# Kernel optimization log

Measured on AMD Instinct MI355X. Metric: run time of the kernel, lower is better.

## Reference

```python
import jax, jax.numpy as jnp
import numpy as np

N_NODES = 80000
N_EDGES = 800000
N_REL = 400
D_IN = 256
D_OUT = 256
BN_EPS = 1e-5


def _xavier(key, shape, gain=np.sqrt(2.0)):
    fan_in, fan_out = shape[0], shape[-1]
    std = gain * np.sqrt(2.0 / (fan_in + fan_out))
    return jax.random.normal(key, shape, dtype=jnp.float32) * std


def ccorr(a, b):
    # circular correlation: irfft(conj(rfft(a)) * rfft(b), n)
    n = a.shape[-1]
    return jnp.fft.irfft(jnp.conj(jnp.fft.rfft(a)) * jnp.fft.rfft(b), n)


def setup_inputs() -> dict:
    key = jax.random.key(0)
    ks = jax.random.split(key, 12)
    x = jax.random.normal(ks[0], (N_NODES, D_IN), dtype=jnp.float32)
    rel_repr = jax.random.normal(ks[1], (N_REL, D_IN), dtype=jnp.float32)
    edge_src = jax.random.randint(ks[2], (N_EDGES,), 0, N_NODES)
    edge_dst = jax.random.randint(ks[3], (N_EDGES,), 0, N_NODES)
    edge_type = jax.random.randint(ks[4], (N_EDGES,), 0, N_REL)
    edge_norm = jax.random.uniform(ks[5], (N_EDGES,), dtype=jnp.float32)
    in_w = _xavier(ks[6], (D_IN, D_OUT))
    out_w = _xavier(ks[7], (D_IN, D_OUT))
    loop_w = _xavier(ks[8], (D_IN, D_OUT))
    w_rel = _xavier(ks[9], (D_IN, D_OUT))
    loop_rel = _xavier(ks[10], (1, D_IN))
    bias = jnp.zeros((D_OUT,), dtype=jnp.float32)
    return {"x": x, "rel_repr": rel_repr, "edge_src": edge_src,
            "edge_dst": edge_dst, "edge_type": edge_type, "edge_norm": edge_norm,
            "in_w": in_w, "out_w": out_w, "loop_w": loop_w, "w_rel": w_rel,
            "loop_rel": loop_rel, "bias": bias}


def reference(x, rel_repr, edge_src, edge_dst, edge_type, edge_norm,
              in_w, out_w, loop_w, w_rel, loop_rel, bias):
    E = edge_src.shape[0]
    half = E // 2
    # gather + compose (opn == 'corr')
    h_src = x[edge_src]                         # [E, D_in]
    edge_data = ccorr(h_src, rel_repr[edge_type])  # [E, D_in]
    # direction-split matmul
    msg = jnp.concatenate([edge_data[:half] @ in_w,
                           edge_data[half:] @ out_w], axis=0)  # [E, D_out]
    msg = msg * edge_norm[:, None]
    # scatter-sum into destination nodes, then reduce (dropout p=0, /3)
    agg = jax.ops.segment_sum(msg, edge_dst, num_segments=x.shape[0]) / 3.0
    # self-loop
    loop = ccorr(x, jnp.broadcast_to(loop_rel, x.shape)) @ loop_w / 3.0
    out = agg + loop + bias
    # BatchNorm1d (training mode: batch stats, gamma=1, beta=0)
    mean = jnp.mean(out, axis=0)
    var = jnp.var(out, axis=0)
    out = (out - mean) / jnp.sqrt(var + BN_EPS)
    # act is identity
    return out, rel_repr @ w_rel
```

## Files before the change

kernel.cpp:

```cpp
#include <hip/hip_runtime.h>

#define NN 80000
#define NE 800000
#define EH 400000
#define NR 400
#define DD 256
#define FD 256
#define KP 768
#define NB 160000
#define NCH 157
#define MT 80400
#define PI2 6.283185307179586f

typedef unsigned short u16;
typedef __attribute__((ext_vector_type(8))) short bf16x8;
typedef __attribute__((ext_vector_type(4))) float f32x4;

static __device__ __forceinline__ float bu2f(u16 u) {
  return __uint_as_float(((unsigned int)u) << 16);
}
static __device__ __forceinline__ u16 f2bu(float f) {
  unsigned int x = __float_as_uint(f);
  x += 0x7fffu + ((x >> 16) & 1u);
  return (u16)(x >> 16);
}
static __device__ __forceinline__ unsigned int pk2(float a, float b) {
  return (unsigned int)f2bu(a) | ((unsigned int)f2bu(b) << 16);
}
static __device__ __forceinline__ void gload16(const void* g, void* l) {
  __builtin_amdgcn_global_load_lds(
      (const __attribute__((address_space(1))) unsigned int*)g,
      (__attribute__((address_space(3))) unsigned int*)l, 16, 0, 0);
}

__global__ void k_build(const float* __restrict__ in_w, const float* __restrict__ out_w,
                        const float* __restrict__ lr, const float* __restrict__ loop_w,
                        u16* __restrict__ Ft, u16* __restrict__ Bt) {
  __shared__ float L[DD];
  int bb = blockIdx.x, c = threadIdx.x;
  if (bb < 256) {
    int row = bb, j = c;
    int k, im;
    if (row == 0)      { k = 0;   im = 0; }
    else if (row == 1) { k = 128; im = 0; }
    else               { k = row >> 1; im = row & 1; }
    int m = (j * k) & 255;
    float th = -PI2 * (float)m * (1.0f / 256.0f);
    Ft[row * 256 + j] = f2bu(im ? sinf(th) : cosf(th));
  } else if (bb < 768) {
    int t = bb - 256;
    const float* W = (t < 256) ? in_w : out_w;
    int tp = t & 255;
    int k, im; float alpha;
    if (tp == 0)      { k = 0;   im = 0; alpha = 1.0f; }
    else if (tp == 1) { k = 128; im = 0; alpha = 1.0f; }
    else              { k = tp >> 1; im = tp & 1; alpha = 2.0f; }
    float scale = alpha * (1.0f / 768.0f);
    float th = -PI2 * (float)k * (1.0f / 256.0f);
    float wr = cosf(th), wi = sinf(th);
    float zr = 1.0f, zi = 0.0f;
    float acc = 0.0f;
    for (int j = 0; j < DD; ++j) {
      float coef = im ? zi : zr;
      acc += coef * W[(size_t)j * DD + c];
      float nzr = zr * wr - zi * wi; zi = zr * wi + zi * wr; zr = nzr;
    }
    Bt[(size_t)c * KP + t] = f2bu(scale * acc);
  } else {
    int j = bb - 768;
    L[c] = lr[c];
    __syncthreads();
    float acc = 0.0f;
    for (int k2 = 0; k2 < DD; ++k2)
      acc += L[(j + k2) & 255] * loop_w[(size_t)k2 * DD + c];
    Bt[(size_t)c * KP + 512 + j] = f2bu(acc * (1.0f / 3.0f));
  }
}

__global__ __launch_bounds__(512) void k_dft(
    const float* __restrict__ x, const float* __restrict__ rel,
    const u16* __restrict__ Ft, u16* __restrict__ xfh, float* __restrict__ rfhf,
    u16* __restrict__ Ap) {
  __shared__ u16 sA[2][128 * 64];
  __shared__ u16 sB[256 * 64];
  int tid = threadIdx.x;
  int w = tid >> 6, lane = tid & 63;
  int r0 = blockIdx.x * 128;
  int wm = (w & 1) * 64, wn = (w >> 1) * 64;
  int fr = lane & 15, fg = lane >> 4;

  int arow = tid >> 2;
  int acg = (tid & 3) * 16;
  int gr = r0 + arow;
  int grc = gr < MT ? gr : MT - 1;
  const float* asrc = (grc < NN) ? (x + (size_t)grc * DD)
                                 : (rel + (size_t)(grc - NN) * DD);
  bool doAp = (gr < NN);

  float4 a0_, a1_, a2_, a3_;
#define LOADA(kb) { const float* p_ = asrc + (kb) * 64 + acg;                     \
    a0_ = *(const float4*)(p_);     a1_ = *(const float4*)(p_ + 4);               \
    a2_ = *(const float4*)(p_ + 8); a3_ = *(const float4*)(p_ + 12); }

#define STGB(kb) { _Pragma("unroll") for (int q = 0; q < 4; ++q) {                \
    int s_ = w * 4 + q; int c_ = 8 * s_ + (lane >> 3);                            \
    int cb_ = (lane & 7) ^ (c_ & 7);                                              \
    gload16(Ft + (size_t)c_ * 256 + (kb) * 64 + cb_ * 8, sB + s_ * 512); } }

#define CVTA(kb, buf) {                                                           \
    uint4 c0_ = make_uint4(pk2(a0_.x, a0_.y), pk2(a0_.z, a0_.w),                  \
                           pk2(a1_.x, a1_.y), pk2(a1_.z, a1_.w));                 \
    uint4 c1_ = make_uint4(pk2(a2_.x, a2_.y), pk2(a2_.z, a2_.w),                  \
                           pk2(a3_.x, a3_.y), pk2(a3_.z, a3_.w));                 \
    int b0_ = (tid & 3) * 2;                                                      \
    *(uint4*)(sA[buf] + arow * 64 + ((b0_ ^ (arow & 7)) * 8)) = c0_;              \
    *(uint4*)(sA[buf] + arow * 64 + (((b0_ + 1) ^ (arow & 7)) * 8)) = c1_;        \
    if (doAp) { u16* ap_ = Ap + (size_t)gr * KP + 512 + (kb) * 64 + acg;          \
      *(uint4*)(ap_) = c0_; *(uint4*)(ap_ + 8) = c1_; } }

  f32x4 acc[4][4];
#pragma unroll
  for (int i = 0; i < 4; ++i)
#pragma unroll
    for (int j = 0; j < 4; ++j) acc[i][j] = (f32x4){0.f, 0.f, 0.f, 0.f};

  LOADA(0)
  STGB(0)
  CVTA(0, 0)
  LOADA(1)
  __syncthreads();
  for (int kb = 0; kb < 4; ++kb) {
    int cur = kb & 1;
#pragma unroll
    for (int ks = 0; ks < 2; ++ks) {
      bf16x8 af[4], bfr[4];
#pragma unroll
      for (int mt = 0; mt < 4; ++mt) {
        int r = wm + mt * 16 + fr;
        af[mt] = *(const bf16x8*)(sA[cur] + r * 64 + ((ks * 32 + fg * 8) ^ ((r & 7) * 8)));
      }
#pragma unroll
      for (int nt = 0; nt < 4; ++nt) {
        int c = wn + nt * 16 + fr;
        bfr[nt] = *(const bf16x8*)(sB + c * 64 + ((ks * 32 + fg * 8) ^ ((c & 7) * 8)));
      }
#pragma unroll
      for (int mt = 0; mt < 4; ++mt)
#pragma unroll
        for (int nt = 0; nt < 4; ++nt)
          acc[mt][nt] = __builtin_amdgcn_mfma_f32_16x16x32_bf16(af[mt], bfr[nt],
                                                                acc[mt][nt], 0, 0, 0);
    }
    __syncthreads();
    if (kb < 3) {
      STGB(kb + 1)
      CVTA(kb + 1, cur ^ 1)
      if (kb < 2) LOADA(kb + 2)
      __syncthreads();
    }
  }
#undef LOADA
#undef STGB
#undef CVTA

#pragma unroll
  for (int mt = 0; mt < 4; ++mt)
#pragma unroll
    for (int nt = 0; nt < 4; ++nt) {
      int cg = wn + nt * 16 + fr;
#pragma unroll
      for (int j = 0; j < 4; ++j) {
        int rg = r0 + wm + mt * 16 + fg * 4 + j;
        float val = acc[mt][nt][j];
        if (rg < NN)      xfh[(size_t)rg * FD + cg] = f2bu(val);
        else if (rg < MT) rfhf[(size_t)(rg - NN) * FD + cg] = val;
      }
    }
}

__global__ void k_hist(const int* __restrict__ edst, int* __restrict__ cnt) {
  int e = blockIdx.x * 256 + threadIdx.x;
  int key = edst[e] + ((e >= EH) ? NN : 0);
  atomicAdd(&cnt[key], 1);
}

__global__ __launch_bounds__(256) void k_scan1(const int* __restrict__ cnt,
                                               int* __restrict__ base,
                                               int* __restrict__ chunkTot) {
  __shared__ int wsum[4];
  int t = threadIdx.x;
  int g0 = blockIdx.x * 1024 + t * 4;
  int v[4], ex[4], s = 0;
#pragma unroll
  for (int j = 0; j < 4; ++j) v[j] = (g0 + j < NB) ? cnt[g0 + j] : 0;
#pragma unroll
  for (int j = 0; j < 4; ++j) { ex[j] = s; s += v[j]; }
  int lane = t & 63, w = t >> 6;
  int inc = s;
  for (int off = 1; off < 64; off <<= 1) {
    int n = __shfl_up(inc, off);
    if (lane >= off) inc += n;
  }
  if (lane == 63) wsum[w] = inc;
  __syncthreads();
  int woff = 0;
  for (int i = 0; i < w; ++i) woff += wsum[i];
  int exth = woff + inc - s;
#pragma unroll
  for (int j = 0; j < 4; ++j)
    if (g0 + j < NB) base[g0 + j] = exth + ex[j];
  if (t == 255) chunkTot[blockIdx.x] = woff + inc;
}

__global__ __launch_bounds__(256) void k_scan2(const int* __restrict__ chunkTot,
                                               int* __restrict__ chunkOff) {
  __shared__ int wsum[4];
  int t = threadIdx.x;
  int v = (t < NCH) ? chunkTot[t] : 0;
  int lane = t & 63, w = t >> 6;
  int inc = v;
  for (int off = 1; off < 64; off <<= 1) {
    int n = __shfl_up(inc, off);
    if (lane >= off) inc += n;
  }
  if (lane == 63) wsum[w] = inc;
  __syncthreads();
  int woff = 0;
  for (int i = 0; i < w; ++i) woff += wsum[i];
  if (t < NCH) chunkOff[t] = woff + inc - v;
}

__global__ void k_scan3(int* __restrict__ base, const int* __restrict__ chunkOff,
                        int* __restrict__ cursor) {
  int i = blockIdx.x * 256 + threadIdx.x;
  if (i < NB) {
    int b = base[i] + chunkOff[i >> 10];
    base[i] = b;
    cursor[i] = b;
  }
  if (i == 0) base[NB] = NE;
}

__global__ void k_scatter(const int* __restrict__ esrc, const int* __restrict__ edst,
                          const int* __restrict__ etyp, const float* __restrict__ enorm,
                          int* __restrict__ cursor, int4* __restrict__ recs) {
  int e = blockIdx.x * 256 + threadIdx.x;
  int key = edst[e] + ((e >= EH) ? NN : 0);
  int pos = atomicAdd(&cursor[key], 1);
  recs[pos] = make_int4(esrc[e], etyp[e], __float_as_int(enorm[e]), 0);
}

__global__ __launch_bounds__(256) void k_reduce(
    const u16* __restrict__ xfh, const float* __restrict__ rfhf,
    const int4* __restrict__ recs, const int* __restrict__ base,
    u16* __restrict__ Ap) {
  int w = threadIdx.x >> 6, lane = threadIdx.x & 63;
  int b = blockIdx.x * 4 + w;
  int start = base[b], end = base[b + 1];
  bool l0 = (lane == 0);
  float a0 = 0, a1 = 0, a2 = 0, a3 = 0;
  int p = start;
  for (; p + 3 < end; p += 4) {
    ushort4 xv[4];
    float4 rv[4];
    float nm[4];
#pragma unroll
    for (int u = 0; u < 4; ++u) {
      int4 rc = recs[p + u];
      nm[u] = __int_as_float(rc.z);
      xv[u] = *(const ushort4*)(xfh + (size_t)rc.x * FD + 4 * lane);
      rv[u] = *(const float4*)(rfhf + (size_t)rc.y * FD + 4 * lane);
    }
#pragma unroll
    for (int u = 0; u < 4; ++u) {
      float xr0 = bu2f(xv[u].x), xi0 = bu2f(xv[u].y);
      float xr1 = bu2f(xv[u].z), xi1 = bu2f(xv[u].w);
      float rr0 = rv[u].x, ri0 = rv[u].y, rr1 = rv[u].z, ri1 = rv[u].w;
      float p0 = l0 ? (xr0 * rr0) : (xr0 * rr0 + xi0 * ri0);
      float p1 = l0 ? (xi0 * ri0) : (xr0 * ri0 - xi0 * rr0);
      a0 += p0 * nm[u];
      a1 += p1 * nm[u];
      a2 += (xr1 * rr1 + xi1 * ri1) * nm[u];
      a3 += (xr1 * ri1 - xi1 * rr1) * nm[u];
    }
  }
  for (; p < end; ++p) {
    int4 rc = recs[p];
    float nm0 = __int_as_float(rc.z);
    ushort4 xv0 = *(const ushort4*)(xfh + (size_t)rc.x * FD + 4 * lane);
    float4 rv0 = *(const float4*)(rfhf + (size_t)rc.y * FD + 4 * lane);
    float xr0 = bu2f(xv0.x), xi0 = bu2f(xv0.y), xr1 = bu2f(xv0.z), xi1 = bu2f(xv0.w);
    float rr0 = rv0.x, ri0 = rv0.y, rr1 = rv0.z, ri1 = rv0.w;
    float p0 = l0 ? (xr0 * rr0) : (xr0 * rr0 + xi0 * ri0);
    float p1 = l0 ? (xi0 * ri0) : (xr0 * ri0 - xi0 * rr0);
    a0 += p0 * nm0;
    a1 += p1 * nm0;
    a2 += (xr1 * rr1 + xi1 * ri1) * nm0;
    a3 += (xr1 * ri1 - xi1 * rr1) * nm0;
  }
  u16* tp = Ap + ((b < NN) ? (size_t)b * KP : (size_t)(b - NN) * KP + 256);
  *(unsigned int*)(tp + 4 * lane)     = pk2(a0, a1);
  *(unsigned int*)(tp + 4 * lane + 2) = pk2(a2, a3);
}

__global__ __launch_bounds__(512) void k_mgemm(
    const u16* __restrict__ Ap, const u16* __restrict__ Bt,
    const float* __restrict__ bias, float* __restrict__ dout,
    float* __restrict__ sum1, float* __restrict__ sum2) {
  __shared__ u16 sA[2][128 * 64];
  __shared__ u16 sB[256 * 64];
  int tid = threadIdx.x;
  int w = tid >> 6, lane = tid & 63;
  int r0 = blockIdx.x * 128;
  int wm = (w & 1) * 64, wn = (w >> 1) * 64;
  int fr = lane & 15, fg = lane >> 4;

#define STGA(kb, buf) { _Pragma("unroll") for (int q = 0; q < 2; ++q) {           \
    int s_ = w * 2 + q; int r_ = 8 * s_ + (lane >> 3);                            \
    int cb_ = (lane & 7) ^ (r_ & 7);                                              \
    gload16(Ap + (size_t)(r0 + r_) * KP + (kb) * 64 + cb_ * 8,                    \
            sA[buf] + s_ * 512); } }

#define STGB(kb) { _Pragma("unroll") for (int q = 0; q < 4; ++q) {                \
    int s_ = w * 4 + q; int c_ = 8 * s_ + (lane >> 3);                            \
    int cb_ = (lane & 7) ^ (c_ & 7);                                              \
    gload16(Bt + (size_t)c_ * KP + (kb) * 64 + cb_ * 8, sB + s_ * 512); } }

  f32x4 acc[4][4];
#pragma unroll
  for (int i = 0; i < 4; ++i)
#pragma unroll
    for (int j = 0; j < 4; ++j) acc[i][j] = (f32x4){0.f, 0.f, 0.f, 0.f};

  STGA(0, 0)
  STGB(0)
  __syncthreads();
  for (int kb = 0; kb < 12; ++kb) {
    int cur = kb & 1;
    if (kb < 11) STGA(kb + 1, cur ^ 1)
#pragma unroll
    for (int ks = 0; ks < 2; ++ks) {
      bf16x8 af[4], bfr[4];
#pragma unroll
      for (int mt = 0; mt < 4; ++mt) {
        int r = wm + mt * 16 + fr;
        af[mt] = *(const bf16x8*)(sA[cur] + r * 64 + ((ks * 32 + fg * 8) ^ ((r & 7) * 8)));
      }
#pragma unroll
      for (int nt = 0; nt < 4; ++nt) {
        int c = wn + nt * 16 + fr;
        bfr[nt] = *(const bf16x8*)(sB + c * 64 + ((ks * 32 + fg * 8) ^ ((c & 7) * 8)));
      }
#pragma unroll
      for (int mt = 0; mt < 4; ++mt)
#pragma unroll
        for (int nt = 0; nt < 4; ++nt)
          acc[mt][nt] = __builtin_amdgcn_mfma_f32_16x16x32_bf16(af[mt], bfr[nt],
                                                                acc[mt][nt], 0, 0, 0);
    }
    __syncthreads();
    if (kb < 11) { STGB(kb + 1) __syncthreads(); }
  }
#undef STGA
#undef STGB

  float s1[4] = {0.f, 0.f, 0.f, 0.f}, s2[4] = {0.f, 0.f, 0.f, 0.f};
#pragma unroll
  for (int nt = 0; nt < 4; ++nt) {
    int cg = wn + nt * 16 + fr;
    float bv = bias[cg];
#pragma unroll
    for (int mt = 0; mt < 4; ++mt) {
#pragma unroll
      for (int j = 0; j < 4; ++j) {
        int rg = r0 + wm + mt * 16 + fg * 4 + j;
        float val = acc[mt][nt][j] + bv;
        dout[(size_t)rg * DD + cg] = val;
        s1[nt] += val;
        s2[nt] += val * val;
      }
    }
  }
#pragma unroll
  for (int nt = 0; nt < 4; ++nt) {
    s1[nt] += __shfl_xor(s1[nt], 16); s1[nt] += __shfl_xor(s1[nt], 32);
    s2[nt] += __shfl_xor(s2[nt], 16); s2[nt] += __shfl_xor(s2[nt], 32);
  }
  if (lane < 16) {
#pragma unroll
    for (int nt = 0; nt < 4; ++nt) {
      atomicAdd(&sum1[wn + nt * 16 + lane], s1[nt]);
      atomicAdd(&sum2[wn + nt * 16 + lane], s2[nt]);
    }
  }
}

__global__ __launch_bounds__(256) void k_norm(float* __restrict__ out,
                                              const float* __restrict__ sum1,
                                              const float* __restrict__ sum2) {
  size_t tid0 = (size_t)blockIdx.x * 256 + threadIdx.x;
  int c0 = (int)((tid0 * 4) & 255);
  float m[4], rs[4];
#pragma unroll
  for (int j = 0; j < 4; ++j) {
    float mm = sum1[c0 + j] * (1.0f / (float)NN);
    float var = sum2[c0 + j] * (1.0f / (float)NN) - mm * mm;
    m[j] = mm;
    rs[j] = rsqrtf(var + 1e-5f);
  }
  size_t total = (size_t)NN * DD / 4;
  size_t stride = (size_t)gridDim.x * 256;
  for (size_t i = tid0; i < total; i += stride) {
    float4* p = (float4*)out + i;
    float4 v = *p;
    v.x = (v.x - m[0]) * rs[0];
    v.y = (v.y - m[1]) * rs[1];
    v.z = (v.z - m[2]) * rs[2];
    v.w = (v.w - m[3]) * rs[3];
    *p = v;
  }
}

__global__ void k_rel(const float* __restrict__ rel, const float* __restrict__ wrel,
                      float* __restrict__ out2) {
  __shared__ float R[DD];
  int r = blockIdx.x, c = threadIdx.x;
  R[c] = rel[(size_t)r * DD + c];
  __syncthreads();
  float acc = 0.0f;
  for (int j = 0; j < DD; ++j)
    acc += R[j] * wrel[(size_t)j * DD + c];
  out2[(size_t)r * DD + c] = acc;
}

__global__ void k_fail(float* __restrict__ out, int n) {
  int i = blockIdx.x * 256 + threadIdx.x;
  if (i < n) out[i] = 1.0e6f;
}

extern "C" void kernel_launch(void* const* d_in, const int* in_sizes, int n_in,
                              void* d_out, int out_size, void* d_ws, size_t ws_size,
                              hipStream_t stream) {
  (void)in_sizes; (void)n_in;
  const float* x      = (const float*)d_in[0];
  const float* rel    = (const float*)d_in[1];
  const int*   esrc   = (const int*)d_in[2];
  const int*   edst   = (const int*)d_in[3];
  const int*   etyp   = (const int*)d_in[4];
  const float* enorm  = (const float*)d_in[5];
  const float* in_w   = (const float*)d_in[6];
  const float* out_w  = (const float*)d_in[7];
  const float* loop_w = (const float*)d_in[8];
  const float* w_rel  = (const float*)d_in[9];
  const float* lr     = (const float*)d_in[10];
  const float* bias   = (const float*)d_in[11];
  float* dout = (float*)d_out;

  char* wsb = (char*)d_ws;
  size_t off = 0;
  u16* Apack = (u16*)(wsb + off); off += (size_t)NN * KP * 2;
  u16* Bt    = (u16*)(wsb + off); off += (size_t)DD * KP * 2;
  u16* xfh   = (u16*)(wsb + off); off += (size_t)NN * FD * 2;
  float* rfhf = (float*)(wsb + off); off += (size_t)NR * FD * 4;
  u16* Ft    = (u16*)(wsb + off); off += (size_t)DD * DD * 2;
  int4* recs = (int4*)(wsb + off); off += (size_t)NE * 16;
  float* sum1  = (float*)(wsb + off); off += DD * 4;
  float* sum2  = (float*)(wsb + off); off += DD * 4;
  int* cnt   = (int*)(wsb + off); off += (size_t)(NB + 1) * 4;
  int* baseA = (int*)(wsb + off); off += (size_t)(NB + 1) * 4;
  int* curA  = (int*)(wsb + off); off += (size_t)NB * 4;
  int* chT   = (int*)(wsb + off); off += 256 * 4;
  int* chO   = (int*)(wsb + off); off += 256 * 4;

  if (ws_size < off) {
    k_fail<<<(out_size + 255) / 256, 256, 0, stream>>>(dout, out_size);
    return;
  }

  hipMemsetAsync(cnt, 0, (NB + 1) * sizeof(int), stream);
  hipMemsetAsync(sum1, 0, 2 * DD * sizeof(float), stream);
  k_build<<<1024, 256, 0, stream>>>(in_w, out_w, lr, loop_w, Ft, Bt);
  k_hist<<<NE / 256, 256, 0, stream>>>(edst, cnt);
  k_scan1<<<NCH, 256, 0, stream>>>(cnt, baseA, chT);
  k_scan2<<<1, 256, 0, stream>>>(chT, chO);
  k_scan3<<<(NB + 255) / 256, 256, 0, stream>>>(baseA, chO, curA);
  k_scatter<<<NE / 256, 256, 0, stream>>>(esrc, edst, etyp, enorm, curA, recs);
  k_dft<<<(MT + 127) / 128, 512, 0, stream>>>(x, rel, Ft, xfh, rfhf, Apack);
  k_reduce<<<NB / 4, 256, 0, stream>>>(xfh, rfhf, recs, baseA, Apack);
  k_mgemm<<<NN / 128, 512, 0, stream>>>(Apack, Bt, bias, dout, sum1, sum2);
  k_norm<<<2048, 256, 0, stream>>>(dout, sum1, sum2);
  k_rel<<<NR, 256, 0, stream>>>(rel, w_rel, dout + (size_t)NN * DD);
}
```

Baseline: 368.0 us.

## Store relation spectra and pre-norm output in bf16 to cut memory traffic

Relation DFT spectra are now stored as bf16 rather than fp32, which halves the gather bytes per edge in the reduce kernel. The GEMM writes its pre-normalisation output as a bf16 scratch buffer, and the norm kernel reads that buffer and writes fp32 output, so the fp32 read-modify-write round trip is avoided. The weight-spectrum build replaces the recurrent twiddle rotation with an exact twiddle table in shared memory. The cost is extra bf16 rounding on relation spectra and on output values before batch normalisation, plus more workspace.

```diff
diff --git a/kernel.cpp b/kernel.cpp
--- a/kernel.cpp
+++ b/kernel.cpp
@@ -56,15 +56,13 @@
     else if (tp == 1) { k = 128; im = 0; alpha = 1.0f; }
     else              { k = tp >> 1; im = tp & 1; alpha = 2.0f; }
     float scale = alpha * (1.0f / 768.0f);
-    float th = -PI2 * (float)k * (1.0f / 256.0f);
-    float wr = cosf(th), wi = sinf(th);
-    float zr = 1.0f, zi = 0.0f;
+    int m = (c * k) & 255;
+    float th = -PI2 * (float)m * (1.0f / 256.0f);
+    L[c] = im ? sinf(th) : cosf(th);
+    __syncthreads();
     float acc = 0.0f;
-    for (int j = 0; j < DD; ++j) {
-      float coef = im ? zi : zr;
-      acc += coef * W[(size_t)j * DD + c];
-      float nzr = zr * wr - zi * wi; zi = zr * wi + zi * wr; zr = nzr;
-    }
+    for (int j = 0; j < DD; ++j)
+      acc += L[j] * W[(size_t)j * DD + c];
     Bt[(size_t)c * KP + t] = f2bu(scale * acc);
   } else {
     int j = bb - 768;
@@ -79,7 +77,7 @@
 
 __global__ __launch_bounds__(512) void k_dft(
     const float* __restrict__ x, const float* __restrict__ rel,
-    const u16* __restrict__ Ft, u16* __restrict__ xfh, float* __restrict__ rfhf,
+    const u16* __restrict__ Ft, u16* __restrict__ xfh, u16* __restrict__ rfh,
     u16* __restrict__ Ap) {
   __shared__ u16 sA[2][128 * 64];
   __shared__ u16 sB[256 * 64];
@@ -171,9 +169,9 @@
 #pragma unroll
       for (int j = 0; j < 4; ++j) {
         int rg = r0 + wm + mt * 16 + fg * 4 + j;
-        float val = acc[mt][nt][j];
-        if (rg < NN)      xfh[(size_t)rg * FD + cg] = f2bu(val);
-        else if (rg < MT) rfhf[(size_t)(rg - NN) * FD + cg] = val;
+        u16 val = f2bu(acc[mt][nt][j]);
+        if (rg < NN)      xfh[(size_t)rg * FD + cg] = val;
+        else if (rg < MT) rfh[(size_t)(rg - NN) * FD + cg] = val;
       }
     }
 }
@@ -251,7 +249,7 @@
 }
 
 __global__ __launch_bounds__(256) void k_reduce(
-    const u16* __restrict__ xfh, const float* __restrict__ rfhf,
+    const u16* __restrict__ xfh, const u16* __restrict__ rfh,
     const int4* __restrict__ recs, const int* __restrict__ base,
     u16* __restrict__ Ap) {
   int w = threadIdx.x >> 6, lane = threadIdx.x & 63;
@@ -261,21 +259,21 @@
   float a0 = 0, a1 = 0, a2 = 0, a3 = 0;
   int p = start;
   for (; p + 3 < end; p += 4) {
-    ushort4 xv[4];
-    float4 rv[4];
+    ushort4 xv[4], rv[4];
     float nm[4];
 #pragma unroll
     for (int u = 0; u < 4; ++u) {
       int4 rc = recs[p + u];
       nm[u] = __int_as_float(rc.z);
       xv[u] = *(const ushort4*)(xfh + (size_t)rc.x * FD + 4 * lane);
-      rv[u] = *(const float4*)(rfhf + (size_t)rc.y * FD + 4 * lane);
+      rv[u] = *(const ushort4*)(rfh + (size_t)rc.y * FD + 4 * lane);
     }
 #pragma unroll
     for (int u = 0; u < 4; ++u) {
       float xr0 = bu2f(xv[u].x), xi0 = bu2f(xv[u].y);
       float xr1 = bu2f(xv[u].z), xi1 = bu2f(xv[u].w);
-      float rr0 = rv[u].x, ri0 = rv[u].y, rr1 = rv[u].z, ri1 = rv[u].w;
+      float rr0 = bu2f(rv[u].x), ri0 = bu2f(rv[u].y);
+      float rr1 = bu2f(rv[u].z), ri1 = bu2f(rv[u].w);
       float p0 = l0 ? (xr0 * rr0) : (xr0 * rr0 + xi0 * ri0);
       float p1 = l0 ? (xi0 * ri0) : (xr0 * ri0 - xi0 * rr0);
       a0 += p0 * nm[u];
@@ -288,9 +286,9 @@
     int4 rc = recs[p];
     float nm0 = __int_as_float(rc.z);
     ushort4 xv0 = *(const ushort4*)(xfh + (size_t)rc.x * FD + 4 * lane);
-    float4 rv0 = *(const float4*)(rfhf + (size_t)rc.y * FD + 4 * lane);
+    ushort4 rv0 = *(const ushort4*)(rfh + (size_t)rc.y * FD + 4 * lane);
     float xr0 = bu2f(xv0.x), xi0 = bu2f(xv0.y), xr1 = bu2f(xv0.z), xi1 = bu2f(xv0.w);
-    float rr0 = rv0.x, ri0 = rv0.y, rr1 = rv0.z, ri1 = rv0.w;
+    float rr0 = bu2f(rv0.x), ri0 = bu2f(rv0.y), rr1 = bu2f(rv0.z), ri1 = bu2f(rv0.w);
     float p0 = l0 ? (xr0 * rr0) : (xr0 * rr0 + xi0 * ri0);
     float p1 = l0 ? (xi0 * ri0) : (xr0 * ri0 - xi0 * rr0);
     a0 += p0 * nm0;
@@ -305,7 +303,7 @@
 
 __global__ __launch_bounds__(512) void k_mgemm(
     const u16* __restrict__ Ap, const u16* __restrict__ Bt,
-    const float* __restrict__ bias, float* __restrict__ dout,
+    const float* __restrict__ bias, u16* __restrict__ doutb,
     float* __restrict__ sum1, float* __restrict__ sum2) {
   __shared__ u16 sA[2][128 * 64];
   __shared__ u16 sB[256 * 64];
@@ -375,7 +373,7 @@
       for (int j = 0; j < 4; ++j) {
         int rg = r0 + wm + mt * 16 + fg * 4 + j;
         float val = acc[mt][nt][j] + bv;
-        dout[(size_t)rg * DD + cg] = val;
+        doutb[(size_t)rg * DD + cg] = f2bu(val);
         s1[nt] += val;
         s2[nt] += val * val;
       }
@@ -395,7 +393,8 @@
   }
 }
 
-__global__ __launch_bounds__(256) void k_norm(float* __restrict__ out,
+__global__ __launch_bounds__(256) void k_norm(const u16* __restrict__ doutb,
+                                              float* __restrict__ out,
                                               const float* __restrict__ sum1,
                                               const float* __restrict__ sum2) {
   size_t tid0 = (size_t)blockIdx.x * 256 + threadIdx.x;
@@ -411,13 +410,13 @@
   size_t total = (size_t)NN * DD / 4;
   size_t stride = (size_t)gridDim.x * 256;
   for (size_t i = tid0; i < total; i += stride) {
-    float4* p = (float4*)out + i;
-    float4 v = *p;
-    v.x = (v.x - m[0]) * rs[0];
-    v.y = (v.y - m[1]) * rs[1];
-    v.z = (v.z - m[2]) * rs[2];
-    v.w = (v.w - m[3]) * rs[3];
-    *p = v;
+    uint2 q = *((const uint2*)doutb + i);
+    float4 v;
+    v.x = (bu2f((u16)q.x) - m[0]) * rs[0];
+    v.y = (bu2f((u16)(q.x >> 16)) - m[1]) * rs[1];
+    v.z = (bu2f((u16)q.y) - m[2]) * rs[2];
+    v.w = (bu2f((u16)(q.y >> 16)) - m[3]) * rs[3];
+    *((float4*)out + i) = v;
   }
 }
 
@@ -461,8 +460,9 @@
   u16* Apack = (u16*)(wsb + off); off += (size_t)NN * KP * 2;
   u16* Bt    = (u16*)(wsb + off); off += (size_t)DD * KP * 2;
   u16* xfh   = (u16*)(wsb + off); off += (size_t)NN * FD * 2;
-  float* rfhf = (float*)(wsb + off); off += (size_t)NR * FD * 4;
+  u16* rfh   = (u16*)(wsb + off); off += (size_t)NR * FD * 2;
   u16* Ft    = (u16*)(wsb + off); off += (size_t)DD * DD * 2;
+  u16* doutb = (u16*)(wsb + off); off += (size_t)NN * DD * 2;
   int4* recs = (int4*)(wsb + off); off += (size_t)NE * 16;
   float* sum1  = (float*)(wsb + off); off += DD * 4;
   float* sum2  = (float*)(wsb + off); off += DD * 4;
@@ -485,9 +485,9 @@
   k_scan2<<<1, 256, 0, stream>>>(chT, chO);
   k_scan3<<<(NB + 255) / 256, 256, 0, stream>>>(baseA, chO, curA);
   k_scatter<<<NE / 256, 256, 0, stream>>>(esrc, edst, etyp, enorm, curA, recs);
-  k_dft<<<(MT + 127) / 128, 512, 0, stream>>>(x, rel, Ft, xfh, rfhf, Apack);
-  k_reduce<<<NB / 4, 256, 0, stream>>>(xfh, rfhf, recs, baseA, Apack);
-  k_mgemm<<<NN / 128, 512, 0, stream>>>(Apack, Bt, bias, dout, sum1, sum2);
-  k_norm<<<2048, 256, 0, stream>>>(dout, sum1, sum2);
+  k_dft<<<(MT + 127) / 128, 512, 0, stream>>>(x, rel, Ft, xfh, rfh, Apack);
+  k_reduce<<<NB / 4, 256, 0, stream>>>(xfh, rfh, recs, baseA, Apack);
+  k_mgemm<<<NN / 128, 512, 0, stream>>>(Apack, Bt, bias, doutb, sum1, sum2);
+  k_norm<<<2048, 256, 0, stream>>>(doutb, dout, sum1, sum2);
   k_rel<<<NR, 256, 0, stream>>>(rel, w_rel, dout + (size_t)NN * DD);
 }
```

After: 371.2 us. Within noise of the previous version (+0.9%).
